# Kernel tuning notes

Hardware: AMD Instinct MI355X
Metric: run time of the kernel (lower is better)

Reference implementation:

```python
import jax, jax.numpy as jnp
import numpy as np

B, C, H, W = 64, 64, 56, 56
MID = 2 * C  # two output nodes concatenated
EPS = 1e-5


def _conv1x1(x, w):
    # x: [B,C,H,W], w: [O,C] (1x1 conv kernel squeezed)
    return jnp.einsum('bchw,oc->bohw', x, w)


def _bn(x, g, b, m, v):
    # eval-mode BatchNorm2d with running stats
    sc = g * jax.lax.rsqrt(v + EPS)
    return x * sc[None, :, None, None] + (b - m * sc)[None, :, None, None]


def _maxpool3(x):
    # MaxPool2d(kernel=3, stride=1, padding=1)
    return jax.lax.reduce_window(x, -jnp.inf, jax.lax.max,
                                 (1, 1, 3, 3), (1, 1, 1, 1),
                                 [(0, 0), (0, 0), (1, 1), (1, 1)])


def _avgpool3(x):
    # AvgPool2d(kernel=3, stride=1, padding=1), count_include_pad=True -> /9
    s = jax.lax.reduce_window(x, 0.0, jax.lax.add,
                              (1, 1, 3, 3), (1, 1, 1, 1),
                              [(0, 0), (0, 0), (1, 1), (1, 1)])
    return s * (1.0 / 9.0)


def setup_inputs() -> dict:
    key = jax.random.key(0)
    ks = jax.random.split(key, 11)
    x = jax.random.normal(ks[0], (B, C, H, W), dtype=jnp.float32)
    w1 = jax.random.normal(ks[1], (C, C), dtype=jnp.float32) * 0.1
    w2 = jax.random.normal(ks[2], (C, MID), dtype=jnp.float32) * 0.1
    bn1_g = 1.0 + 0.1 * jax.random.normal(ks[3], (C,), dtype=jnp.float32)
    bn1_b = 0.1 * jax.random.normal(ks[4], (C,), dtype=jnp.float32)
    bn1_m = 0.1 * jax.random.normal(ks[5], (C,), dtype=jnp.float32)
    bn1_v = jax.random.uniform(ks[6], (C,), minval=0.5, maxval=1.5, dtype=jnp.float32)
    bn2_g = 1.0 + 0.1 * jax.random.normal(ks[7], (C,), dtype=jnp.float32)
    bn2_b = 0.1 * jax.random.normal(ks[8], (C,), dtype=jnp.float32)
    bn2_m = 0.1 * jax.random.normal(ks[9], (C,), dtype=jnp.float32)
    bn2_v = jax.random.uniform(ks[10], (C,), minval=0.5, maxval=1.5, dtype=jnp.float32)
    return dict(x=x, w1=w1, w2=w2,
                bn1_g=bn1_g, bn1_b=bn1_b, bn1_m=bn1_m, bn1_v=bn1_v,
                bn2_g=bn2_g, bn2_b=bn2_b, bn2_m=bn2_m, bn2_v=bn2_v)


def reference(x, w1, w2, bn1_g, bn1_b, bn1_m, bn1_v, bn2_g, bn2_b, bn2_m, bn2_v):
    # DAG g = [[[0,1],[1,2]], [[4,3],[3]], [[5,3],[3,100]], [[4,3],[100]]]
    # topoSort order: [0, 2, 1, 3]; output nodes (ordered): [2, 3]
    node0 = jax.nn.relu(_bn(_conv1x1(x, w1), bn1_g, bn1_b, bn1_m, bn1_v))
    node1 = _maxpool3(node0)            # op type 4, pred {0}
    node2 = _avgpool3(node0)            # op type 5, pred {0}
    node3 = _maxpool3(node1) + _maxpool3(node2)  # op type 4, preds {1,2}, summed
    cat = jnp.concatenate([node2, node3], axis=1)  # [B, 2C, H, W]
    out = jax.nn.relu(_bn(_conv1x1(cat, w2), bn2_g, bn2_b, bn2_m, bn2_v))
    return out
```

## Files before the change

kernel.cpp:

```cpp
#include <hip/hip_runtime.h>
#include <cstddef>

#define EPS 1e-5f
static constexpr int Bn = 64, Cn = 64, Hn = 56, Wn = 56, HWn = Hn * Wn;
static constexpr int RB = 8;
static constexpr int NBAND = 7;
static constexpr int SLAB = 3600;

typedef __attribute__((ext_vector_type(8))) short short8;
typedef __attribute__((ext_vector_type(8))) unsigned short ushort8;
typedef __attribute__((ext_vector_type(4))) unsigned short ushort4v;
typedef __attribute__((ext_vector_type(4))) float floatx4;
typedef __attribute__((ext_vector_type(16))) float floatx16;
typedef __attribute__((ext_vector_type(4))) unsigned int uintx4;
typedef __attribute__((ext_vector_type(2))) unsigned int uintx2;

__device__ __forceinline__ unsigned pack_rne(float a, float b) {
    unsigned ua = __float_as_uint(a), ub = __float_as_uint(b);
    ua = ua + 0x7fffu + ((ua >> 16) & 1u);
    ub = ub + 0x7fffu + ((ub >> 16) & 1u);
    return __builtin_amdgcn_perm(ub, ua, 0x07060302);
}
__device__ __forceinline__ unsigned pack_trunc(float a, float b) {
    return __builtin_amdgcn_perm(__float_as_uint(b), __float_as_uint(a), 0x07060302);
}
__device__ __forceinline__ uintx2 pmax2(uintx2 a, uintx2 b) {
    ushort4v r = __builtin_elementwise_max(*(ushort4v*)&a, *(ushort4v*)&b);
    return *(uintx2*)&r;
}
__device__ __forceinline__ float bf_lo(unsigned u) { return __uint_as_float(u << 16); }
__device__ __forceinline__ float bf_hi(unsigned u) { return __uint_as_float(u & 0xffff0000u); }


__global__ __launch_bounds__(256, 2) void k1_conv1(
    const float* __restrict__ x, const float* __restrict__ w1,
    const float* __restrict__ bg, const float* __restrict__ bb,
    const float* __restrict__ bm, const float* __restrict__ bv,
    unsigned short* __restrict__ node0)
{
    __shared__ float scs[64], shs[64];
    const int tid = threadIdx.x;
    if (tid < 64) {
        float sc = bg[tid] * rsqrtf(bv[tid] + EPS);
        scs[tid] = sc;
        shs[tid] = bb[tid] - bm[tid] * sc;
    }
    __syncthreads();
    const int lane = tid & 63;
    const int wv   = tid >> 6;
    const int n    = lane & 31;
    const int h    = lane >> 5;

    short8 afr0[4], afr1[4];
    {
        const float s0 = scs[n], s1 = scs[32 + n];
        #pragma unroll
        for (int kt = 0; kt < 4; ++kt) {
            const float* wp0 = w1 + (size_t)n * 64 + kt * 16 + h * 8;
            floatx4 f0 = *(const floatx4*)wp0;
            floatx4 f1 = *(const floatx4*)(wp0 + 4);
            uintx4 u;
            u.x = pack_rne(f0[0] * s0, f0[1] * s0);
            u.y = pack_rne(f0[2] * s0, f0[3] * s0);
            u.z = pack_rne(f1[0] * s0, f1[1] * s0);
            u.w = pack_rne(f1[2] * s0, f1[3] * s0);
            afr0[kt] = *(short8*)&u;
            const float* wp1 = wp0 + 32 * 64;
            floatx4 g0 = *(const floatx4*)wp1;
            floatx4 g1 = *(const floatx4*)(wp1 + 4);
            uintx4 v;
            v.x = pack_rne(g0[0] * s1, g0[1] * s1);
            v.y = pack_rne(g0[2] * s1, g0[3] * s1);
            v.z = pack_rne(g1[0] * s1, g1[1] * s1);
            v.w = pack_rne(g1[2] * s1, g1[3] * s1);
            afr1[kt] = *(short8*)&v;
        }
    }

    const int P = blockIdx.x * 256 + wv * 64;
    const int b = P / HWn, p0 = P - b * HWn;
    const float* xb = x + (size_t)b * 64 * HWn + p0 + n;

    float f0[4][8], f1[4][8];
    #pragma unroll
    for (int kt = 0; kt < 4; ++kt)
        #pragma unroll
        for (int j = 0; j < 8; ++j) {
            const float* xp = xb + (size_t)(kt * 16 + h * 8 + j) * HWn;
            f0[kt][j] = xp[0];
            f1[kt][j] = xp[32];
        }

    #pragma unroll
    for (int s = 0; s < 2; ++s) {
        floatx16 acc0, acc1;
        #pragma unroll
        for (int i = 0; i < 16; ++i) { acc0[i] = 0.f; acc1[i] = 0.f; }

        #pragma unroll
        for (int kt = 0; kt < 4; ++kt) {
            float* fr = s ? f1[kt] : f0[kt];
            uintx4 u;
            u.x = pack_trunc(fr[0], fr[1]);
            u.y = pack_trunc(fr[2], fr[3]);
            u.z = pack_trunc(fr[4], fr[5]);
            u.w = pack_trunc(fr[6], fr[7]);
            short8 bfr = *(short8*)&u;
            acc0 = __builtin_amdgcn_mfma_f32_32x32x16_bf16(afr0[kt], bfr, acc0, 0, 0, 0);
            acc1 = __builtin_amdgcn_mfma_f32_32x32x16_bf16(afr1[kt], bfr, acc1, 0, 0, 0);
        }

        #pragma unroll
        for (int oct = 0; oct < 2; ++oct) {
            #pragma unroll
            for (int g = 0; g < 4; ++g) {
                floatx4 sh4 = *(const floatx4*)&shs[oct * 32 + g * 8 + h * 4];
                float v0 = (oct ? acc1[g * 4 + 0] : acc0[g * 4 + 0]) + sh4[0]; v0 = v0 > 0.f ? v0 : 0.f;
                float v1 = (oct ? acc1[g * 4 + 1] : acc0[g * 4 + 1]) + sh4[1]; v1 = v1 > 0.f ? v1 : 0.f;
                float v2 = (oct ? acc1[g * 4 + 2] : acc0[g * 4 + 2]) + sh4[2]; v2 = v2 > 0.f ? v2 : 0.f;
                float v3 = (oct ? acc1[g * 4 + 3] : acc0[g * 4 + 3]) + sh4[3]; v3 = v3 > 0.f ? v3 : 0.f;
                uintx2 st;
                st.x = pack_rne(v0, v1);
                st.y = pack_rne(v2, v3);
                const int chunk = oct * 4 + g;
                *(uintx2*)(node0 + ((size_t)(b * 8 + chunk) * HWn + p0 + s * 32 + n) * 8 + h * 4) = st;
            }
        }
    }
}

__global__ __launch_bounds__(1024, 4) void k23_fused(
    const unsigned short* __restrict__ node0,
    const float* __restrict__ w2,
    const float* __restrict__ bg, const float* __restrict__ bb,
    const float* __restrict__ bm, const float* __restrict__ bv,
    float* __restrict__ out)
{
    __shared__ __align__(16) unsigned short catl[16 * SLAB];
    const int tid = threadIdx.x;
    const int lane = tid & 63;
    const int wv = tid >> 6;

    const int bid = blockIdx.x;
    const int xcd = bid & 7;
    const int jj = bid >> 3;
    const int b = xcd * 8 + jj / NBAND;
    const int band = jj % NBAND;
    const int lo = band * RB;

    {
        const int chunk = wv >> 1;
        const int c0 = (wv & 1) * 28;
        const int local = lane >> 1;
        const int col = c0 - 2 + local;
        const int jh = lane & 1;
        const unsigned short* base = node0 + ((size_t)(b * 8 + chunk) * HWn) * 8 + jh * 4;

        const uintx2 zz = (uintx2){0u, 0u};
        auto loadrow = [&](int r) -> uintx2 {
            if (((unsigned)col >= (unsigned)Wn) | ((unsigned)r >= (unsigned)Hn)) return zz;
            return *(const uintx2*)(base + (size_t)(r * Wn + col) * 8);
        };

        float hs1[4], hs2[4];
        #pragma unroll
        for (int c = 0; c < 4; ++c) hs1[c] = hs2[c] = 0.f;
        uintx2 h5a = zz, h5b = zz, h5c = zz, h5d = zz, nh1 = zz, nh2 = zz;

        uintx2 cur = loadrow(lo - 2);
        uintx2 nxt = loadrow(lo - 1);

        unsigned short* cav = catl + (size_t)(chunk * 2) * SLAB + jh * 4;
        unsigned short* cmx = cav + SLAB;
        const bool stcol = (local >= 2) & (local <= 29);

        #pragma unroll
        for (int i = 0; i < RB + 4; ++i) {
            const int r = lo - 2 + i;
            uintx2 nx2 = (i < RB + 2) ? loadrow(r + 2) : zz;

            uintx2 D0, D1, D3, D4;
            #pragma unroll
            for (int w = 0; w < 2; ++w) {
                unsigned u = cur[w];
                D1[w] = __shfl_up(u, 2);
                D0[w] = __shfl_up(u, 4);
                D3[w] = __shfl_down(u, 2);
                D4[w] = __shfl_down(u, 4);
            }

            uintx2 hm5 = pmax2(pmax2(pmax2(D0, D1), pmax2(cur, D3)), D4);
            uintx2 m5 = pmax2(pmax2(pmax2(h5a, h5b), pmax2(h5c, h5d)), hm5);
            h5a = h5b; h5b = h5c; h5c = h5d; h5d = hm5;

            float a2[4];
            #pragma unroll
            for (int w = 0; w < 2; ++w) {
                float s0 = bf_lo(D1[w]) + bf_lo(cur[w]) + bf_lo(D3[w]);
                float s1 = bf_hi(D1[w]) + bf_hi(cur[w]) + bf_hi(D3[w]);
                a2[w * 2 + 0] = (hs2[w * 2 + 0] + hs1[w * 2 + 0] + s0) * (1.f / 9.f);
                a2[w * 2 + 1] = (hs2[w * 2 + 1] + hs1[w * 2 + 1] + s1) * (1.f / 9.f);
                hs2[w * 2 + 0] = hs1[w * 2 + 0]; hs1[w * 2 + 0] = s0;
                hs2[w * 2 + 1] = hs1[w * 2 + 1]; hs1[w * 2 + 1] = s1;
            }
            uintx2 ap;
            ap.x = pack_rne(a2[0], a2[1]);
            ap.y = pack_rne(a2[2], a2[3]);

            uintx2 al, ar;
            #pragma unroll
            for (int w = 0; w < 2; ++w) {
                al[w] = __shfl_up(ap[w], 2);
                ar[w] = __shfl_down(ap[w], 2);
            }
            uintx2 nh = pmax2(pmax2(al, ap), ar);
            uintx2 m3 = pmax2(pmax2(nh2, nh1), nh);
            nh2 = nh1; nh1 = nh;

            const int r2 = r - 1, r3 = r - 2;
            if (stcol && i >= 3 && i <= RB + 2)
                *(uintx2*)(cav + (size_t)((r2 - lo) * Wn + col) * 8) = ap;
            if (stcol && i >= 4) {
                uintx2 st;
                st.x = pack_rne(bf_lo(m5.x) + bf_lo(m3.x), bf_hi(m5.x) + bf_hi(m3.x));
                st.y = pack_rne(bf_lo(m5.y) + bf_lo(m3.y), bf_hi(m5.y) + bf_hi(m3.y));
                *(uintx2*)(cmx + (size_t)((r3 - lo) * Wn + col) * 8) = st;
            }
            cur = nxt; nxt = nx2;
        }
    }

    const int m16 = lane & 15;
    const int q = lane >> 4;
    const int t = wv & 3;
    const int e = wv >> 2;
    short8 afr[4];
    #pragma unroll
    for (int cp = 0; cp < 4; ++cp) {
        const int c = 2 * cp + (q >> 1);
        const int chb = ((q & 1) ? 64 : 0) + 8 * c;
        const float* wp = w2 + (size_t)(t * 16 + m16) * 128 + chb;
        floatx4 f0 = *(const floatx4*)wp;
        floatx4 f1 = *(const floatx4*)(wp + 4);
        uintx4 u;
        u.x = pack_rne(f0[0], f0[1]);
        u.y = pack_rne(f0[2], f0[3]);
        u.z = pack_rne(f1[0], f1[1]);
        u.w = pack_rne(f1[2], f1[3]);
        afr[cp] = *(short8*)&u;
    }
    const int oc0 = t * 16 + q * 4;
    floatx4 g4 = *(const floatx4*)(bg + oc0);
    floatx4 bb4 = *(const floatx4*)(bb + oc0);
    floatx4 mm4 = *(const floatx4*)(bm + oc0);
    floatx4 vv4 = *(const floatx4*)(bv + oc0);
    float sc[4], sh[4];
    #pragma unroll
    for (int r = 0; r < 4; ++r) {
        sc[r] = g4[r] * rsqrtf(vv4[r] + EPS);
        sh[r] = bb4[r] - mm4[r] * sc[r];
    }
    __syncthreads();

    floatx4 acc[7];
    #pragma unroll
    for (int i = 0; i < 7; ++i) acc[i] = (floatx4){0.f, 0.f, 0.f, 0.f};

    #pragma unroll
    for (int cp = 0; cp < 4; ++cp) {
        #pragma unroll
        for (int i = 0; i < 7; ++i) {
            const int px = (e * 7 + i) * 16 + m16;
            short8 bfr = *(const short8*)(catl + (size_t)(4 * cp + q) * SLAB + (size_t)px * 8);
            acc[i] = __builtin_amdgcn_mfma_f32_16x16x32_bf16(afr[cp], bfr, acc[i], 0, 0, 0);
        }
    }

    float* ob = out + (size_t)(b * 64 + oc0) * HWn + lo * Wn;
    #pragma unroll
    for (int i = 0; i < 7; ++i) {
        const int px = (e * 7 + i) * 16 + m16;
        #pragma unroll
        for (int r = 0; r < 4; ++r) {
            float v = fmaf(acc[i][r], sc[r], sh[r]);
            ob[(size_t)r * HWn + px] = v > 0.f ? v : 0.f;
        }
    }
}

extern "C" void kernel_launch(void* const* d_in, const int* in_sizes, int n_in,
                              void* d_out, int out_size, void* d_ws, size_t ws_size,
                              hipStream_t stream)
{
    const float* x   = (const float*)d_in[0];
    const float* w1  = (const float*)d_in[1];
    const float* w2  = (const float*)d_in[2];
    const float* b1g = (const float*)d_in[3];
    const float* b1b = (const float*)d_in[4];
    const float* b1m = (const float*)d_in[5];
    const float* b1v = (const float*)d_in[6];
    const float* b2g = (const float*)d_in[7];
    const float* b2b = (const float*)d_in[8];
    const float* b2m = (const float*)d_in[9];
    const float* b2v = (const float*)d_in[10];

    float* out = (float*)d_out;
    unsigned short* node0 = (unsigned short*)d_ws;

    k1_conv1<<<dim3(784), dim3(256), 0, stream>>>(x, w1, b1g, b1b, b1m, b1v, node0);
    k23_fused<<<dim3(Bn * NBAND), dim3(1024), 0, stream>>>(node0, w2, b2g, b2b, b2m, b2v, out);
}
```

Baseline: 149.8 us.

## Split fused pool+conv2 band into two LDS phases to shrink shared memory

The fused pooling and second-conv kernel now processes each 7-row band in two sub-passes of at most 4 rows. Each sub-pass recomputes its halo rows and shares a smaller LDS slab, which roughly halves shared memory per block and raises launch bounds so more blocks can be resident. The cost is redundant halo loads and pooling work, an extra barrier pair, and a rolled loop with a tail MFMA guard. The first kernel also gets an XCD-aware block remap and a higher occupancy hint.

```diff
diff --git a/kernel.cpp b/kernel.cpp
--- a/kernel.cpp
+++ b/kernel.cpp
@@ -3,12 +3,11 @@
 
 #define EPS 1e-5f
 static constexpr int Bn = 64, Cn = 64, Hn = 56, Wn = 56, HWn = Hn * Wn;
-static constexpr int RB = 8;
-static constexpr int NBAND = 7;
-static constexpr int SLAB = 3600;
+static constexpr int RB = 7;
+static constexpr int NBAND = 8;
+static constexpr int SLAB = 1808;
 
 typedef __attribute__((ext_vector_type(8))) short short8;
-typedef __attribute__((ext_vector_type(8))) unsigned short ushort8;
 typedef __attribute__((ext_vector_type(4))) unsigned short ushort4v;
 typedef __attribute__((ext_vector_type(4))) float floatx4;
 typedef __attribute__((ext_vector_type(16))) float floatx16;
@@ -32,7 +31,7 @@
 __device__ __forceinline__ float bf_hi(unsigned u) { return __uint_as_float(u & 0xffff0000u); }
 
 
-__global__ __launch_bounds__(256, 2) void k1_conv1(
+__global__ __launch_bounds__(256, 3) void k1_conv1(
     const float* __restrict__ x, const float* __restrict__ w1,
     const float* __restrict__ bg, const float* __restrict__ bb,
     const float* __restrict__ bm, const float* __restrict__ bv,
@@ -77,7 +76,10 @@
         }
     }
 
-    const int P = blockIdx.x * 256 + wv * 64;
+    const int bid = blockIdx.x;
+    const int xcd = bid & 7;
+    const int idx = bid >> 3;
+    const int P = (xcd * 98 + idx) * 256 + wv * 64;
     const int b = P / HWn, p0 = P - b * HWn;
     const float* xb = x + (size_t)b * 64 * HWn + p0 + n;
 
@@ -129,7 +131,7 @@
     }
 }
 
-__global__ __launch_bounds__(1024, 4) void k23_fused(
+__global__ __launch_bounds__(1024, 8) void k23_fused(
     const unsigned short* __restrict__ node0,
     const float* __restrict__ w2,
     const float* __restrict__ bg, const float* __restrict__ bb,
@@ -144,91 +146,21 @@
     const int bid = blockIdx.x;
     const int xcd = bid & 7;
     const int jj = bid >> 3;
-    const int b = xcd * 8 + jj / NBAND;
-    const int band = jj % NBAND;
+    const int b = xcd * 8 + (jj >> 3);
+    const int band = jj & 7;
     const int lo = band * RB;
 
-    {
-        const int chunk = wv >> 1;
-        const int c0 = (wv & 1) * 28;
-        const int local = lane >> 1;
-        const int col = c0 - 2 + local;
-        const int jh = lane & 1;
-        const unsigned short* base = node0 + ((size_t)(b * 8 + chunk) * HWn) * 8 + jh * 4;
-
-        const uintx2 zz = (uintx2){0u, 0u};
-        auto loadrow = [&](int r) -> uintx2 {
-            if (((unsigned)col >= (unsigned)Wn) | ((unsigned)r >= (unsigned)Hn)) return zz;
-            return *(const uintx2*)(base + (size_t)(r * Wn + col) * 8);
-        };
-
-        float hs1[4], hs2[4];
-        #pragma unroll
-        for (int c = 0; c < 4; ++c) hs1[c] = hs2[c] = 0.f;
-        uintx2 h5a = zz, h5b = zz, h5c = zz, h5d = zz, nh1 = zz, nh2 = zz;
-
-        uintx2 cur = loadrow(lo - 2);
-        uintx2 nxt = loadrow(lo - 1);
-
-        unsigned short* cav = catl + (size_t)(chunk * 2) * SLAB + jh * 4;
-        unsigned short* cmx = cav + SLAB;
-        const bool stcol = (local >= 2) & (local <= 29);
-
-        #pragma unroll
-        for (int i = 0; i < RB + 4; ++i) {
-            const int r = lo - 2 + i;
-            uintx2 nx2 = (i < RB + 2) ? loadrow(r + 2) : zz;
-
-            uintx2 D0, D1, D3, D4;
-            #pragma unroll
-            for (int w = 0; w < 2; ++w) {
-                unsigned u = cur[w];
-                D1[w] = __shfl_up(u, 2);
-                D0[w] = __shfl_up(u, 4);
-                D3[w] = __shfl_down(u, 2);
-                D4[w] = __shfl_down(u, 4);
-            }
-
-            uintx2 hm5 = pmax2(pmax2(pmax2(D0, D1), pmax2(cur, D3)), D4);
-            uintx2 m5 = pmax2(pmax2(pmax2(h5a, h5b), pmax2(h5c, h5d)), hm5);
-            h5a = h5b; h5b = h5c; h5c = h5d; h5d = hm5;
-
-            float a2[4];
-            #pragma unroll
-            for (int w = 0; w < 2; ++w) {
-                float s0 = bf_lo(D1[w]) + bf_lo(cur[w]) + bf_lo(D3[w]);
-                float s1 = bf_hi(D1[w]) + bf_hi(cur[w]) + bf_hi(D3[w]);
-                a2[w * 2 + 0] = (hs2[w * 2 + 0] + hs1[w * 2 + 0] + s0) * (1.f / 9.f);
-                a2[w * 2 + 1] = (hs2[w * 2 + 1] + hs1[w * 2 + 1] + s1) * (1.f / 9.f);
-                hs2[w * 2 + 0] = hs1[w * 2 + 0]; hs1[w * 2 + 0] = s0;
-                hs2[w * 2 + 1] = hs1[w * 2 + 1]; hs1[w * 2 + 1] = s1;
-            }
-            uintx2 ap;
-            ap.x = pack_rne(a2[0], a2[1]);
-            ap.y = pack_rne(a2[2], a2[3]);
-
-            uintx2 al, ar;
-            #pragma unroll
-            for (int w = 0; w < 2; ++w) {
-                al[w] = __shfl_up(ap[w], 2);
-                ar[w] = __shfl_down(ap[w], 2);
-            }
-            uintx2 nh = pmax2(pmax2(al, ap), ar);
-            uintx2 m3 = pmax2(pmax2(nh2, nh1), nh);
-            nh2 = nh1; nh1 = nh;
-
-            const int r2 = r - 1, r3 = r - 2;
-            if (stcol && i >= 3 && i <= RB + 2)
-                *(uintx2*)(cav + (size_t)((r2 - lo) * Wn + col) * 8) = ap;
-            if (stcol && i >= 4) {
-                uintx2 st;
-                st.x = pack_rne(bf_lo(m5.x) + bf_lo(m3.x), bf_hi(m5.x) + bf_hi(m3.x));
-                st.y = pack_rne(bf_lo(m5.y) + bf_lo(m3.y), bf_hi(m5.y) + bf_hi(m3.y));
-                *(uintx2*)(cmx + (size_t)((r3 - lo) * Wn + col) * 8) = st;
-            }
-            cur = nxt; nxt = nx2;
-        }
-    }
+    const int chunk = wv >> 1;
+    const int c0 = (wv & 1) * 28;
+    const int local = lane >> 1;
+    const int col = c0 - 2 + local;
+    const int jh = lane & 1;
+    const bool colok = (unsigned)col < (unsigned)Wn;
+    const bool stcol = (local >= 2) & (local <= 29);
+    const unsigned short* base = node0 + ((size_t)(b * 8 + chunk) * HWn) * 8 + jh * 4;
+    unsigned short* cav = catl + (size_t)(chunk * 2) * SLAB + jh * 4;
+    unsigned short* cmx = cav + SLAB;
+    const uintx2 zz = (uintx2){0u, 0u};
 
     const int m16 = lane & 15;
     const int q = lane >> 4;
@@ -254,37 +186,108 @@
     floatx4 bb4 = *(const floatx4*)(bb + oc0);
     floatx4 mm4 = *(const floatx4*)(bm + oc0);
     floatx4 vv4 = *(const floatx4*)(bv + oc0);
-    float sc[4], sh[4];
+    float sc2[4], sh2[4];
     #pragma unroll
     for (int r = 0; r < 4; ++r) {
-        sc[r] = g4[r] * rsqrtf(vv4[r] + EPS);
-        sh[r] = bb4[r] - mm4[r] * sc[r];
-    }
-    __syncthreads();
-
-    floatx4 acc[7];
-    #pragma unroll
-    for (int i = 0; i < 7; ++i) acc[i] = (floatx4){0.f, 0.f, 0.f, 0.f};
-
-    #pragma unroll
-    for (int cp = 0; cp < 4; ++cp) {
-        #pragma unroll
-        for (int i = 0; i < 7; ++i) {
-            const int px = (e * 7 + i) * 16 + m16;
-            short8 bfr = *(const short8*)(catl + (size_t)(4 * cp + q) * SLAB + (size_t)px * 8);
-            acc[i] = __builtin_amdgcn_mfma_f32_16x16x32_bf16(afr[cp], bfr, acc[i], 0, 0, 0);
-        }
-    }
-
-    float* ob = out + (size_t)(b * 64 + oc0) * HWn + lo * Wn;
-    #pragma unroll
-    for (int i = 0; i < 7; ++i) {
-        const int px = (e * 7 + i) * 16 + m16;
-        #pragma unroll
-        for (int r = 0; r < 4; ++r) {
-            float v = fmaf(acc[i][r], sc[r], sh[r]);
-            ob[(size_t)r * HWn + px] = v > 0.f ? v : 0.f;
-        }
+        sc2[r] = g4[r] * rsqrtf(vv4[r] + EPS);
+        sh2[r] = bb4[r] - mm4[r] * sc2[r];
+    }
+    float* ob = out + (size_t)(b * 64 + oc0) * HWn;
+
+    for (int p = 0; p < 2; ++p) {
+        const int lop = lo + 4 * p;
+        const int nr = p ? (RB - 4) : 4;
+
+        {
+            auto loadrow = [&](int r) -> uintx2 {
+                if ((!colok) | ((unsigned)r >= (unsigned)Hn)) return zz;
+                return *(const uintx2*)(base + (size_t)(r * Wn + col) * 8);
+            };
+            float hs1[4], hs2[4];
+            #pragma unroll
+            for (int c = 0; c < 4; ++c) hs1[c] = hs2[c] = 0.f;
+            uintx2 h5a = zz, h5b = zz, h5c = zz, h5d = zz, nh1 = zz, nh2 = zz;
+
+            uintx2 cur = loadrow(lop - 2);
+            uintx2 nxt = loadrow(lop - 1);
+
+            for (int i = 0; i < nr + 4; ++i) {
+                const int r = lop - 2 + i;
+                uintx2 nx2 = (i < nr + 2) ? loadrow(r + 2) : zz;
+
+                uintx2 D0, D1, D3, D4;
+                #pragma unroll
+                for (int w = 0; w < 2; ++w) {
+                    unsigned u = cur[w];
+                    D1[w] = __shfl_up(u, 2);
+                    D0[w] = __shfl_up(u, 4);
+                    D3[w] = __shfl_down(u, 2);
+                    D4[w] = __shfl_down(u, 4);
+                }
+
+                uintx2 hm5 = pmax2(pmax2(pmax2(D0, D1), pmax2(cur, D3)), D4);
+                uintx2 m5 = pmax2(pmax2(pmax2(h5a, h5b), pmax2(h5c, h5d)), hm5);
+                h5a = h5b; h5b = h5c; h5c = h5d; h5d = hm5;
+
+                float a2[4];
+                #pragma unroll
+                for (int w = 0; w < 2; ++w) {
+                    float s0 = bf_lo(D1[w]) + bf_lo(cur[w]) + bf_lo(D3[w]);
+                    float s1 = bf_hi(D1[w]) + bf_hi(cur[w]) + bf_hi(D3[w]);
+                    a2[w * 2 + 0] = (hs2[w * 2 + 0] + hs1[w * 2 + 0] + s0) * (1.f / 9.f);
+                    a2[w * 2 + 1] = (hs2[w * 2 + 1] + hs1[w * 2 + 1] + s1) * (1.f / 9.f);
+                    hs2[w * 2 + 0] = hs1[w * 2 + 0]; hs1[w * 2 + 0] = s0;
+                    hs2[w * 2 + 1] = hs1[w * 2 + 1]; hs1[w * 2 + 1] = s1;
+                }
+                uintx2 ap;
+                ap.x = pack_rne(a2[0], a2[1]);
+                ap.y = pack_rne(a2[2], a2[3]);
+
+                uintx2 al, ar;
+                #pragma unroll
+                for (int w = 0; w < 2; ++w) {
+                    al[w] = __shfl_up(ap[w], 2);
+                    ar[w] = __shfl_down(ap[w], 2);
+                }
+                uintx2 nh = pmax2(pmax2(al, ap), ar);
+                uintx2 m3 = pmax2(pmax2(nh2, nh1), nh);
+                nh2 = nh1; nh1 = nh;
+
+                const int r2 = r - 1, r3 = r - 2;
+                if (stcol && i >= 3 && i <= nr + 2)
+                    *(uintx2*)(cav + (size_t)((r2 - lop) * Wn + col) * 8) = ap;
+                if (stcol && i >= 4) {
+                    uintx2 st;
+                    st.x = pack_rne(bf_lo(m5.x) + bf_lo(m3.x), bf_hi(m5.x) + bf_hi(m3.x));
+                    st.y = pack_rne(bf_lo(m5.y) + bf_lo(m3.y), bf_hi(m5.y) + bf_hi(m3.y));
+                    *(uintx2*)(cmx + (size_t)((r3 - lop) * Wn + col) * 8) = st;
+                }
+                cur = nxt; nxt = nx2;
+            }
+        }
+        __syncthreads();
+
+        const int npxc = nr * Wn;
+        const int nPT = (npxc + 15) >> 4;
+        for (int k = 0; k < 4; ++k) {
+            const int pt = e + 4 * k;
+            if (pt >= nPT) break;
+            const int px = pt * 16 + m16;
+            floatx4 acc = (floatx4){0.f, 0.f, 0.f, 0.f};
+            #pragma unroll
+            for (int cp = 0; cp < 4; ++cp) {
+                short8 bfr = *(const short8*)(catl + (size_t)(4 * cp + q) * SLAB + (size_t)px * 8);
+                acc = __builtin_amdgcn_mfma_f32_16x16x32_bf16(afr[cp], bfr, acc, 0, 0, 0);
+            }
+            if (px < npxc) {
+                #pragma unroll
+                for (int r = 0; r < 4; ++r) {
+                    float v = fmaf(acc[r], sc2[r], sh2[r]);
+                    ob[(size_t)r * HWn + lop * Wn + px] = v > 0.f ? v : 0.f;
+                }
+            }
+        }
+        __syncthreads();
     }
 }
 
```

Measured after the change: 258.0 us. 72.3% more time.
